# Kernel optimization log

Hardware: AMD Instinct MI355X
Metric: run time of the kernel (lower is better)

Reference implementation:

```python
import jax, jax.numpy as jnp
import numpy as np

N_NODES = 50000
N_EDGES = 800000
IN_CH = 128
HID = 128
NUM_CLASSES = 10
NUM_GRAPHS = 64


def _linear_params(key, fan_in, fan_out):
    kw, kb = jax.random.split(key)
    s = 1.0 / np.sqrt(fan_in)
    W = jax.random.uniform(kw, (fan_in, fan_out), jnp.float32, -s, s)
    b = jax.random.uniform(kb, (fan_out,), jnp.float32, -s, s)
    return W, b


def setup_inputs() -> dict:
    key = jax.random.key(0)
    ks = jax.random.split(key, 16)
    x = jax.random.normal(ks[0], (N_NODES, IN_CH), jnp.float32)
    edge_index = jax.random.randint(ks[1], (2, N_EDGES), 0, N_NODES, jnp.int64)
    batch = jnp.sort(jax.random.randint(ks[2], (N_NODES,), 0, NUM_GRAPHS, jnp.int64))
    inp = {"x": x, "edge_index": edge_index, "batch": batch}
    # conv layer 1 (in -> hid)
    inp["Wk1"], inp["bk1"] = _linear_params(ks[3], IN_CH, HID)
    inp["Wq1"], inp["bq1"] = _linear_params(ks[4], IN_CH, HID)
    inp["Wv1"], inp["bv1"] = _linear_params(ks[5], IN_CH, HID)
    inp["Ws1"], inp["bs1"] = _linear_params(ks[6], IN_CH, HID)
    inp["b1"] = jnp.zeros((HID,), jnp.float32)
    # conv layer 2 (hid -> hid)
    inp["Wk2"], inp["bk2"] = _linear_params(ks[7], HID, HID)
    inp["Wq2"], inp["bq2"] = _linear_params(ks[8], HID, HID)
    inp["Wv2"], inp["bv2"] = _linear_params(ks[9], HID, HID)
    inp["Ws2"], inp["bs2"] = _linear_params(ks[10], HID, HID)
    inp["b2"] = jnp.zeros((HID,), jnp.float32)
    # final fc
    inp["fcW"], inp["fcb"] = _linear_params(ks[11], HID, NUM_CLASSES)
    return inp


def _res_gated_conv(x, src, dst, Wk, bk, Wq, bq, Wv, bv, Ws, bs, b):
    # k from target node i, q and v from source node j (PyG ResGatedGraphConv)
    k = x @ Wk + bk            # [N, H]
    q = x @ Wq + bq            # [N, H]
    v = x @ Wv + bv            # [N, H]
    gate = jax.nn.sigmoid(k[dst] + q[src])   # [E, H]
    msg = gate * v[src]                       # [E, H]
    agg = jax.ops.segment_sum(msg, dst, num_segments=x.shape[0])
    return agg + x @ Ws + bs + b


def _global_mean_pool(x, batch, num_graphs):
    sums = jax.ops.segment_sum(x, batch, num_segments=num_graphs)
    cnts = jax.ops.segment_sum(jnp.ones((x.shape[0],), x.dtype), batch, num_segments=num_graphs)
    return sums / jnp.maximum(cnts, 1.0)[:, None]


def reference(x, edge_index, batch,
              Wk1, bk1, Wq1, bq1, Wv1, bv1, Ws1, bs1, b1,
              Wk2, bk2, Wq2, bq2, Wv2, bv2, Ws2, bs2, b2,
              fcW, fcb):
    src, dst = edge_index[0], edge_index[1]
    h = _res_gated_conv(x, src, dst, Wk1, bk1, Wq1, bq1, Wv1, bv1, Ws1, bs1, b1)
    h = jax.nn.relu(h)
    h = _res_gated_conv(h, src, dst, Wk2, bk2, Wq2, bq2, Wv2, bv2, Ws2, bs2, b2)
    h = jax.nn.relu(h)
    g = _global_mean_pool(h, batch, NUM_GRAPHS)   # [NUM_GRAPHS, HID]
    return g @ fcW + fcb                           # [NUM_GRAPHS, NUM_CLASSES]
```

## Files before the change

### kernel.cpp

```cpp
#include <hip/hip_runtime.h>
#include <math.h>


typedef __attribute__((ext_vector_type(8))) short short8;
typedef __attribute__((ext_vector_type(4))) float floatx4;
typedef __attribute__((ext_vector_type(8))) float floatx8;
typedef __attribute__((ext_vector_type(8))) unsigned short ushort8v;

__device__ __forceinline__ unsigned short f2b(float f) {
  unsigned int u = __builtin_bit_cast(unsigned int, f);
  u += 0x7fff + ((u >> 16) & 1);
  return (unsigned short)(u >> 16);
}
__device__ __forceinline__ float b2f(unsigned short u) {
  return __builtin_bit_cast(float, ((unsigned int)u) << 16);
}


__global__ __launch_bounds__(256) void hist_kernel(const int* __restrict__ dst,
                                                   int* __restrict__ cnt, int E) {
  int e = blockIdx.x * 256 + threadIdx.x;
  if (e < E) atomicAdd(&cnt[dst[e]], 1);
}

__global__ __launch_bounds__(256) void scan1_kernel(const int* __restrict__ cnt,
                                                    int* __restrict__ tmp_excl,
                                                    int* __restrict__ bsum, int n) {
  __shared__ int s[256];
  int t = threadIdx.x;
  int base = blockIdx.x * 512;
  int i0 = base + 2 * t, i1 = i0 + 1;
  int a0 = (i0 < n) ? cnt[i0] : 0;
  int a1 = (i1 < n) ? cnt[i1] : 0;
  int sum = a0 + a1;
  s[t] = sum;
  __syncthreads();
  for (int off = 1; off < 256; off <<= 1) {
    int v = (t >= off) ? s[t - off] : 0;
    __syncthreads();
    s[t] += v;
    __syncthreads();
  }
  int excl = s[t] - sum;
  if (i0 < n) tmp_excl[i0] = excl;
  if (i1 < n) tmp_excl[i1] = excl + a0;
  if (t == 255) bsum[blockIdx.x] = s[255];
}

__global__ __launch_bounds__(128) void scan2_kernel(const int* __restrict__ bsum,
                                                    int* __restrict__ boff, int nb) {
  __shared__ int s[128];
  int t = threadIdx.x;
  int v = (t < nb) ? bsum[t] : 0;
  s[t] = v;
  __syncthreads();
  for (int off = 1; off < 128; off <<= 1) {
    int u = (t >= off) ? s[t - off] : 0;
    __syncthreads();
    s[t] += u;
    __syncthreads();
  }
  if (t < nb) boff[t] = s[t] - v;
}

__global__ __launch_bounds__(256) void finalize_rp_kernel(const int* __restrict__ tmp_excl,
                                                          const int* __restrict__ boff,
                                                          int* __restrict__ row_ptr,
                                                          int* __restrict__ cursor,
                                                          int n, int E) {
  int i = blockIdx.x * 256 + threadIdx.x;
  if (i < n) {
    int v = tmp_excl[i] + boff[i >> 9];
    row_ptr[i] = v;
    cursor[i] = v;
  }
  if (i == 0) row_ptr[n] = E;
}

__global__ __launch_bounds__(256) void scatter_kernel(const int* __restrict__ src,
                                                      const int* __restrict__ dst,
                                                      int* __restrict__ cursor,
                                                      int* __restrict__ es, int E) {
  int e = blockIdx.x * 256 + threadIdx.x;
  if (e < E) {
    int i = dst[e];
    int p = atomicAdd(&cursor[i], 1);
    es[p] = src[e];
  }
}


__global__ __launch_bounds__(256) void convert_kernel(const float* __restrict__ X,
                                                      unsigned short* __restrict__ Xb,
                                                      int total4) {
  int i = blockIdx.x * 256 + threadIdx.x;
  if (i < total4) {
    float4 v = ((const float4*)X)[i];
    ushort4 o;
    o.x = f2b(v.x); o.y = f2b(v.y); o.z = f2b(v.z); o.w = f2b(v.w);
    ((ushort4*)Xb)[i] = o;
  }
}

__global__ __launch_bounds__(256) void prepack_w_kernel(
    const float* __restrict__ Wk1, const float* __restrict__ Wq1,
    const float* __restrict__ Wv1, const float* __restrict__ Ws1,
    const float* __restrict__ Wk2, const float* __restrict__ Wq2,
    const float* __restrict__ Wv2, const float* __restrict__ Ws2,
    unsigned short* __restrict__ WT) {
  int idx = blockIdx.x * 256 + threadIdx.x;
  int layer = idx >> 16;
  int rem = idx & 0xFFFF;
  int mat = rem >> 14;
  int nk = rem & 0x3FFF;
  int nn = nk >> 7, kk = nk & 127;
  int sel = layer * 4 + mat;
  const float* W = (sel == 0) ? Wk1 : (sel == 1) ? Wq1 : (sel == 2) ? Wv1 :
                   (sel == 3) ? Ws1 : (sel == 4) ? Wk2 : (sel == 5) ? Wq2 :
                   (sel == 6) ? Wv2 : Ws2;
  WT[idx] = f2b(W[kk * 128 + nn]);
}

__global__ __launch_bounds__(256) void prepack_b_kernel(
    const float* __restrict__ bk1, const float* __restrict__ bq1,
    const float* __restrict__ bv1, const float* __restrict__ bs1,
    const float* __restrict__ b1,
    const float* __restrict__ bk2, const float* __restrict__ bq2,
    const float* __restrict__ bv2, const float* __restrict__ bs2,
    const float* __restrict__ b2,
    float* __restrict__ bcat) {
  int idx = blockIdx.x * 256 + threadIdx.x;
  if (idx >= 1024) return;
  int layer = idx >> 9;
  int rem = idx & 511;
  int mat = rem >> 7, c = rem & 127;
  int sel = layer * 4 + mat;
  const float* b = (sel == 0) ? bk1 : (sel == 1) ? bq1 : (sel == 2) ? bv1 :
                   (sel == 3) ? bs1 : (sel == 4) ? bk2 : (sel == 5) ? bq2 :
                   (sel == 6) ? bv2 : bs2;
  float v = b[c];
  if (mat == 3) v += (layer == 0) ? b1[c] : b2[c];
  bcat[idx] = v;
}


__global__ __launch_bounds__(256) void gemm_mfma_kernel(
    const unsigned short* __restrict__ Xb,
    const unsigned short* __restrict__ WT,
    const float* __restrict__ bcat,
    unsigned short* __restrict__ Kb, unsigned short* __restrict__ Qb,
    unsigned short* __restrict__ Vb, float* __restrict__ S, int n) {
  __shared__ unsigned short aT[128 * 136];
  __shared__ float estage[4][16 * 68];

  int t = threadIdx.x;
  int row0 = blockIdx.x * 128;
  int m = blockIdx.y;

#pragma unroll
  for (int i = 0; i < 8; ++i) {
    int c = i * 256 + t;
    int r = c >> 4, col16 = c & 15;
    int4 v = make_int4(0, 0, 0, 0);
    if (row0 + r < n) v = *(const int4*)&Xb[(size_t)(row0 + r) * 128 + col16 * 8];
    *(int4*)&aT[r * 136 + col16 * 8] = v;
  }
  __syncthreads();

  int lane = t & 63, wid = t >> 6;
  int wy = wid >> 1, wx = wid & 1;
  int l15 = lane & 15, lq = lane >> 4;

  const unsigned short* WTm = WT + (size_t)m * 16384;

  floatx4 acc[4][4];
#pragma unroll
  for (int mf = 0; mf < 4; ++mf)
#pragma unroll
    for (int nf = 0; nf < 4; ++nf) acc[mf][nf] = (floatx4)(0.0f);

#pragma unroll
  for (int ks = 0; ks < 4; ++ks) {
    int kof = ks * 32 + lq * 8;
    short8 a[4], b[4];
#pragma unroll
    for (int mf = 0; mf < 4; ++mf)
      a[mf] = *(const short8*)&aT[(wy * 64 + mf * 16 + l15) * 136 + kof];
#pragma unroll
    for (int nf = 0; nf < 4; ++nf)
      b[nf] = *(const short8*)&WTm[(size_t)(wx * 64 + nf * 16 + l15) * 128 + kof];
#pragma unroll
    for (int mf = 0; mf < 4; ++mf)
#pragma unroll
      for (int nf = 0; nf < 4; ++nf)
        acc[mf][nf] = __builtin_amdgcn_mfma_f32_16x16x32_bf16(a[mf], b[nf], acc[mf][nf], 0, 0, 0);
  }

  const float* bias = bcat + m * 128;
  int r4 = lane >> 2, cq4 = lane & 3;
  int col = wx * 64 + cq4 * 16;
  float4 bv[4];
#pragma unroll
  for (int j = 0; j < 4; ++j) bv[j] = *(const float4*)&bias[col + j * 4];

  unsigned short* Ob = (m == 0) ? Kb : (m == 1) ? Qb : Vb;

#pragma unroll
  for (int mf = 0; mf < 4; ++mf) {
#pragma unroll
    for (int nf = 0; nf < 4; ++nf)
#pragma unroll
      for (int i = 0; i < 4; ++i)
        estage[wid][(lq * 4 + i) * 68 + nf * 16 + l15] = acc[mf][nf][i];
    int grow = row0 + wy * 64 + mf * 16 + r4;
    if (grow < n) {
      float4 p[4];
#pragma unroll
      for (int j = 0; j < 4; ++j) {
        float4 e = *(const float4*)&estage[wid][r4 * 68 + cq4 * 16 + j * 4];
        p[j].x = e.x + bv[j].x; p[j].y = e.y + bv[j].y;
        p[j].z = e.z + bv[j].z; p[j].w = e.w + bv[j].w;
      }
      if (m < 3) {
        ushort8v o0, o1;
        o0[0] = f2b(p[0].x); o0[1] = f2b(p[0].y); o0[2] = f2b(p[0].z); o0[3] = f2b(p[0].w);
        o0[4] = f2b(p[1].x); o0[5] = f2b(p[1].y); o0[6] = f2b(p[1].z); o0[7] = f2b(p[1].w);
        o1[0] = f2b(p[2].x); o1[1] = f2b(p[2].y); o1[2] = f2b(p[2].z); o1[3] = f2b(p[2].w);
        o1[4] = f2b(p[3].x); o1[5] = f2b(p[3].y); o1[6] = f2b(p[3].z); o1[7] = f2b(p[3].w);
        *(ushort8v*)&Ob[(size_t)grow * 128 + col] = o0;
        *(ushort8v*)&Ob[(size_t)grow * 128 + col + 8] = o1;
      } else {
#pragma unroll
        for (int j = 0; j < 4; ++j)
          *(float4*)&S[(size_t)grow * 128 + col + j * 4] = p[j];
      }
    }
  }
}


__global__ __launch_bounds__(256) void edge_agg_kernel(
    const unsigned short* __restrict__ Kb, const unsigned short* __restrict__ Qb,
    const unsigned short* __restrict__ Vb, const float* __restrict__ S,
    const int* __restrict__ row_ptr, const int* __restrict__ es,
    unsigned short* __restrict__ Hb, float* __restrict__ Hf, int mode, int n) {
  int wid = threadIdx.x >> 6;
  int lane = threadIdx.x & 63;
  int node = blockIdx.x * 4 + wid;
  if (node >= n) return;
  int grp = lane >> 4;
  int l16 = lane & 15;

  ushort8v kr = *(const ushort8v*)&Kb[(size_t)node * 128 + l16 * 8];
  float kc[8];
#pragma unroll
  for (int i = 0; i < 8; ++i) kc[i] = b2f(kr[i]);

  floatx8 acc = (floatx8)(0.0f);

  int e0 = row_ptr[node], e1 = row_ptr[node + 1];
  int e = e0 + grp;
  int j = (e < e1) ? es[e] : -1;
  while (j >= 0) {
    int en = e + 4;
    int jn = (en < e1) ? es[en] : -1;
    ushort8v q8 = *(const ushort8v*)&Qb[(size_t)j * 128 + l16 * 8];
    ushort8v v8 = *(const ushort8v*)&Vb[(size_t)j * 128 + l16 * 8];
#pragma unroll
    for (int i = 0; i < 8; ++i) {
      float q = b2f(q8[i]);
      float v = b2f(v8[i]);
      acc[i] += v / (1.0f + __expf(-(kc[i] + q)));
    }
    e = en; j = jn;
  }

#pragma unroll
  for (int i = 0; i < 8; ++i) {
    acc[i] += __shfl_xor(acc[i], 16);
    acc[i] += __shfl_xor(acc[i], 32);
  }

  if (grp == 0) {
    float4 s0 = *(const float4*)&S[(size_t)node * 128 + l16 * 8];
    float4 s1 = *(const float4*)&S[(size_t)node * 128 + l16 * 8 + 4];
    float r[8];
    r[0] = fmaxf(acc[0] + s0.x, 0.f); r[1] = fmaxf(acc[1] + s0.y, 0.f);
    r[2] = fmaxf(acc[2] + s0.z, 0.f); r[3] = fmaxf(acc[3] + s0.w, 0.f);
    r[4] = fmaxf(acc[4] + s1.x, 0.f); r[5] = fmaxf(acc[5] + s1.y, 0.f);
    r[6] = fmaxf(acc[6] + s1.z, 0.f); r[7] = fmaxf(acc[7] + s1.w, 0.f);
    if (mode == 0) {
      ushort8v o;
#pragma unroll
      for (int i = 0; i < 8; ++i) o[i] = f2b(r[i]);
      *(ushort8v*)&Hb[(size_t)node * 128 + l16 * 8] = o;
    } else {
      float4 h0 = make_float4(r[0], r[1], r[2], r[3]);
      float4 h1 = make_float4(r[4], r[5], r[6], r[7]);
      *(float4*)&Hf[(size_t)node * 128 + l16 * 8] = h0;
      *(float4*)&Hf[(size_t)node * 128 + l16 * 8 + 4] = h1;
    }
  }
}


__global__ __launch_bounds__(64) void graph_bounds_kernel(const int* __restrict__ batch,
                                                          int* __restrict__ gstart, int n) {
  int g = threadIdx.x;
  int lo = 0, hi = n;
  while (lo < hi) {
    int mid = (lo + hi) >> 1;
    if (batch[mid] < g) lo = mid + 1; else hi = mid;
  }
  gstart[g] = lo;
  if (g == 63) gstart[64] = n;
}

__global__ __launch_bounds__(256) void pool_sum_kernel(const float* __restrict__ Hf,
                                                       const int* __restrict__ gstart,
                                                       float* __restrict__ pool) {
  __shared__ float red[8 * 128];
  int g = blockIdx.x >> 4;
  int slice = blockIdx.x & 15;
  int t = threadIdx.x;
  int grp = t >> 5;
  int cq = t & 31;
  int s = gstart[g], e = gstart[g + 1];
  int cnt = e - s;
  int per = (cnt + 15) >> 4;
  int ss = s + slice * per;
  int ee = ss + per; if (ee > e) ee = e;

  float4 acc = make_float4(0.f, 0.f, 0.f, 0.f);
  const float4* H4 = (const float4*)Hf;
  for (int nd = ss + grp; nd < ee; nd += 8) {
    float4 v = H4[(size_t)nd * 32 + cq];
    acc.x += v.x; acc.y += v.y; acc.z += v.z; acc.w += v.w;
  }
  *(float4*)&red[grp * 128 + cq * 4] = acc;
  __syncthreads();
  if (t < 128) {
    float tot = 0.f;
#pragma unroll
    for (int g8 = 0; g8 < 8; ++g8) tot += red[g8 * 128 + t];
    if (tot != 0.f) atomicAdd(&pool[g * 128 + t], tot);
  }
}

__global__ __launch_bounds__(128) void fc_kernel(const float* __restrict__ pool,
                                                 const int* __restrict__ gstart,
                                                 const float* __restrict__ fcW,
                                                 const float* __restrict__ fcb,
                                                 float* __restrict__ out) {
  __shared__ float p[128];
  int g = blockIdx.x;
  int t = threadIdx.x;
  int cnt = gstart[g + 1] - gstart[g];
  float inv = 1.0f / (float)((cnt > 0) ? cnt : 1);
  p[t] = pool[g * 128 + t] * inv;
  __syncthreads();
  if (t < 10) {
    float s = fcb[t];
    for (int c = 0; c < 128; ++c) s += p[c] * fcW[c * 10 + t];
    out[g * 10 + t] = s;
  }
}


extern "C" void kernel_launch(void* const* d_in, const int* in_sizes, int n_in,
                              void* d_out, int out_size, void* d_ws, size_t ws_size,
                              hipStream_t stream) {
  const float* x   = (const float*)d_in[0];
  const int* eidx  = (const int*)d_in[1];
  const int* batch = (const int*)d_in[2];
  const float* Wk1 = (const float*)d_in[3];  const float* bk1 = (const float*)d_in[4];
  const float* Wq1 = (const float*)d_in[5];  const float* bq1 = (const float*)d_in[6];
  const float* Wv1 = (const float*)d_in[7];  const float* bv1 = (const float*)d_in[8];
  const float* Ws1 = (const float*)d_in[9];  const float* bs1 = (const float*)d_in[10];
  const float* b1  = (const float*)d_in[11];
  const float* Wk2 = (const float*)d_in[12]; const float* bk2 = (const float*)d_in[13];
  const float* Wq2 = (const float*)d_in[14]; const float* bq2 = (const float*)d_in[15];
  const float* Wv2 = (const float*)d_in[16]; const float* bv2 = (const float*)d_in[17];
  const float* Ws2 = (const float*)d_in[18]; const float* bs2 = (const float*)d_in[19];
  const float* b2  = (const float*)d_in[20];
  const float* fcW = (const float*)d_in[21]; const float* fcb = (const float*)d_in[22];
  float* out = (float*)d_out;

  const int N = in_sizes[0] / 128;
  const int E = in_sizes[1] / 2;
  const int* src = eidx;
  const int* dst = eidx + E;

  char* w = (char*)d_ws;
  size_t off = 0;
  auto carve = [&](size_t bytes) -> void* {
    void* p = w + off;
    off += (bytes + 255) & ~size_t(255);
    return p;
  };
  const size_t featB16 = (size_t)N * 128 * 2;
  const size_t featB32 = (size_t)N * 128 * 4;
  unsigned short* Xb = (unsigned short*)carve(featB16);
  unsigned short* Kb = (unsigned short*)carve(featB16);
  unsigned short* Qb = (unsigned short*)carve(featB16);
  unsigned short* Vb = (unsigned short*)carve(featB16);
  unsigned short* Hb = (unsigned short*)carve(featB16);
  float* S  = (float*)carve(featB32);
  float* Hf = (float*)carve(featB32);
  unsigned short* WT = (unsigned short*)carve(2 * 4 * 128 * 128 * 2);
  float* bcat = (float*)carve(1024 * 4);
  int* cnt      = (int*)carve((size_t)N * 4);
  int* row_ptr  = (int*)carve((size_t)(N + 1) * 4);
  int* cursor   = (int*)carve((size_t)N * 4);
  int* tmp_excl = (int*)carve((size_t)N * 4);
  int* bsum     = (int*)carve(256 * 4);
  int* boff     = (int*)carve(256 * 4);
  int* es       = (int*)carve((size_t)E * 4);
  int* gstart   = (int*)carve(65 * 4);
  float* pool   = (float*)carve(64 * 128 * 4);
  (void)ws_size; (void)n_in; (void)out_size;

  hipMemsetAsync(cnt, 0, (size_t)N * 4, stream);
  hipMemsetAsync(pool, 0, 64 * 128 * 4, stream);

  int nb512 = (N + 511) / 512;
  hist_kernel<<<(E + 255) / 256, 256, 0, stream>>>(dst, cnt, E);
  scan1_kernel<<<nb512, 256, 0, stream>>>(cnt, tmp_excl, bsum, N);
  scan2_kernel<<<1, 128, 0, stream>>>(bsum, boff, nb512);
  finalize_rp_kernel<<<(N + 255) / 256, 256, 0, stream>>>(tmp_excl, boff, row_ptr, cursor, N, E);
  scatter_kernel<<<(E + 255) / 256, 256, 0, stream>>>(src, dst, cursor, es, E);

  convert_kernel<<<(N * 32 + 255) / 256, 256, 0, stream>>>(x, Xb, N * 32);
  prepack_w_kernel<<<512, 256, 0, stream>>>(Wk1, Wq1, Wv1, Ws1, Wk2, Wq2, Wv2, Ws2, WT);
  prepack_b_kernel<<<4, 256, 0, stream>>>(bk1, bq1, bv1, bs1, b1,
                                          bk2, bq2, bv2, bs2, b2, bcat);

  dim3 ggrid((N + 127) / 128, 4);

  gemm_mfma_kernel<<<ggrid, 256, 0, stream>>>(Xb, WT, bcat, Kb, Qb, Vb, S, N);
  edge_agg_kernel<<<(N + 3) / 4, 256, 0, stream>>>(Kb, Qb, Vb, S, row_ptr, es,
                                                   Hb, Hf, 0, N);

  gemm_mfma_kernel<<<ggrid, 256, 0, stream>>>(Hb, WT + 65536, bcat + 512,
                                              Kb, Qb, Vb, S, N);
  edge_agg_kernel<<<(N + 3) / 4, 256, 0, stream>>>(Kb, Qb, Vb, S, row_ptr, es,
                                                   Hb, Hf, 1, N);

  graph_bounds_kernel<<<1, 64, 0, stream>>>(batch, gstart, N);
  pool_sum_kernel<<<1024, 256, 0, stream>>>(Hf, gstart, pool);
  fc_kernel<<<64, 128, 0, stream>>>(pool, gstart, fcW, fcb, out);
}
```

Measured before the change: 431.7 us.

## Merge prep kernels, drop graph bounds kernel, cheaper sigmoid, reuse LDS for staging

Merges the input conversion and weight/bias prepack kernels into one launch. The graph-bounds kernel is dropped and pool/fc now binary-search the batch array inline. The edge sigmoid uses exp2 with a pre-scaled key and a hardware reciprocal instead of a divide. The GEMM epilogue stages results in the A-tile LDS after a barrier instead of a separate buffer, which lowers LDS use and may raise occupancy. The aim is fewer launches and cheaper per-edge math, at the cost of redundant binary searches and a slightly less accurate reciprocal.

```diff
diff --git a/kernel.cpp b/kernel.cpp
--- a/kernel.cpp
+++ b/kernel.cpp
@@ -6,6 +6,8 @@
 typedef __attribute__((ext_vector_type(4))) float floatx4;
 typedef __attribute__((ext_vector_type(8))) float floatx8;
 typedef __attribute__((ext_vector_type(8))) unsigned short ushort8v;
+
+#define LOG2E 1.4426950408889634f
 
 __device__ __forceinline__ unsigned short f2b(float f) {
   unsigned int u = __builtin_bit_cast(unsigned int, f);
@@ -90,57 +92,61 @@
 }
 
 
-__global__ __launch_bounds__(256) void convert_kernel(const float* __restrict__ X,
-                                                      unsigned short* __restrict__ Xb,
-                                                      int total4) {
-  int i = blockIdx.x * 256 + threadIdx.x;
-  if (i < total4) {
-    float4 v = ((const float4*)X)[i];
-    ushort4 o;
-    o.x = f2b(v.x); o.y = f2b(v.y); o.z = f2b(v.z); o.w = f2b(v.w);
-    ((ushort4*)Xb)[i] = o;
-  }
-}
-
-__global__ __launch_bounds__(256) void prepack_w_kernel(
+__global__ __launch_bounds__(256) void prep_kernel(
+    const float* __restrict__ X, unsigned short* __restrict__ Xb, int total4,
     const float* __restrict__ Wk1, const float* __restrict__ Wq1,
     const float* __restrict__ Wv1, const float* __restrict__ Ws1,
     const float* __restrict__ Wk2, const float* __restrict__ Wq2,
     const float* __restrict__ Wv2, const float* __restrict__ Ws2,
-    unsigned short* __restrict__ WT) {
-  int idx = blockIdx.x * 256 + threadIdx.x;
-  int layer = idx >> 16;
-  int rem = idx & 0xFFFF;
-  int mat = rem >> 14;
-  int nk = rem & 0x3FFF;
-  int nn = nk >> 7, kk = nk & 127;
-  int sel = layer * 4 + mat;
-  const float* W = (sel == 0) ? Wk1 : (sel == 1) ? Wq1 : (sel == 2) ? Wv1 :
-                   (sel == 3) ? Ws1 : (sel == 4) ? Wk2 : (sel == 5) ? Wq2 :
-                   (sel == 6) ? Wv2 : Ws2;
-  WT[idx] = f2b(W[kk * 128 + nn]);
-}
-
-__global__ __launch_bounds__(256) void prepack_b_kernel(
+    unsigned short* __restrict__ WT,
     const float* __restrict__ bk1, const float* __restrict__ bq1,
     const float* __restrict__ bv1, const float* __restrict__ bs1,
     const float* __restrict__ b1,
     const float* __restrict__ bk2, const float* __restrict__ bq2,
     const float* __restrict__ bv2, const float* __restrict__ bs2,
     const float* __restrict__ b2,
-    float* __restrict__ bcat) {
-  int idx = blockIdx.x * 256 + threadIdx.x;
-  if (idx >= 1024) return;
-  int layer = idx >> 9;
-  int rem = idx & 511;
-  int mat = rem >> 7, c = rem & 127;
-  int sel = layer * 4 + mat;
-  const float* b = (sel == 0) ? bk1 : (sel == 1) ? bq1 : (sel == 2) ? bv1 :
-                   (sel == 3) ? bs1 : (sel == 4) ? bk2 : (sel == 5) ? bq2 :
-                   (sel == 6) ? bv2 : bs2;
-  float v = b[c];
-  if (mat == 3) v += (layer == 0) ? b1[c] : b2[c];
-  bcat[idx] = v;
+    float* __restrict__ bcat, int nconvb) {
+  int b = blockIdx.x;
+  if (b < nconvb) {
+    int i = b * 256 + threadIdx.x;
+    if (i < total4) {
+      float4 v = ((const float4*)X)[i];
+      ushort4 o;
+      o.x = f2b(v.x); o.y = f2b(v.y); o.z = f2b(v.z); o.w = f2b(v.w);
+      ((ushort4*)Xb)[i] = o;
+    }
+    return;
+  }
+  b -= nconvb;
+  if (b < 512) {
+    int idx = b * 256 + threadIdx.x;
+    int layer = idx >> 16;
+    int rem = idx & 0xFFFF;
+    int mat = rem >> 14;
+    int nk = rem & 0x3FFF;
+    int nn = nk >> 7, kk = nk & 127;
+    int sel = layer * 4 + mat;
+    const float* W = (sel == 0) ? Wk1 : (sel == 1) ? Wq1 : (sel == 2) ? Wv1 :
+                     (sel == 3) ? Ws1 : (sel == 4) ? Wk2 : (sel == 5) ? Wq2 :
+                     (sel == 6) ? Wv2 : Ws2;
+    WT[idx] = f2b(W[kk * 128 + nn]);
+    return;
+  }
+  b -= 512;
+  {
+    int idx = b * 256 + threadIdx.x;
+    if (idx >= 1024) return;
+    int layer = idx >> 9;
+    int rem = idx & 511;
+    int mat = rem >> 7, c = rem & 127;
+    int sel = layer * 4 + mat;
+    const float* bb = (sel == 0) ? bk1 : (sel == 1) ? bq1 : (sel == 2) ? bv1 :
+                      (sel == 3) ? bs1 : (sel == 4) ? bk2 : (sel == 5) ? bq2 :
+                      (sel == 6) ? bv2 : bs2;
+    float v = bb[c];
+    if (mat == 3) v += (layer == 0) ? b1[c] : b2[c];
+    bcat[idx] = v;
+  }
 }
 
 
@@ -151,7 +157,6 @@
     unsigned short* __restrict__ Kb, unsigned short* __restrict__ Qb,
     unsigned short* __restrict__ Vb, float* __restrict__ S, int n) {
   __shared__ unsigned short aT[128 * 136];
-  __shared__ float estage[4][16 * 68];
 
   int t = threadIdx.x;
   int row0 = blockIdx.x * 128;
@@ -196,6 +201,9 @@
         acc[mf][nf] = __builtin_amdgcn_mfma_f32_16x16x32_bf16(a[mf], b[nf], acc[mf][nf], 0, 0, 0);
   }
 
+  __syncthreads();
+  float* estage = (float*)aT + (size_t)wid * 1088;
+
   const float* bias = bcat + m * 128;
   int r4 = lane >> 2, cq4 = lane & 3;
   int col = wx * 64 + cq4 * 16;
@@ -211,13 +219,13 @@
     for (int nf = 0; nf < 4; ++nf)
 #pragma unroll
       for (int i = 0; i < 4; ++i)
-        estage[wid][(lq * 4 + i) * 68 + nf * 16 + l15] = acc[mf][nf][i];
+        estage[(lq * 4 + i) * 68 + nf * 16 + l15] = acc[mf][nf][i];
     int grow = row0 + wy * 64 + mf * 16 + r4;
     if (grow < n) {
       float4 p[4];
 #pragma unroll
       for (int j = 0; j < 4; ++j) {
-        float4 e = *(const float4*)&estage[wid][r4 * 68 + cq4 * 16 + j * 4];
+        float4 e = *(const float4*)&estage[r4 * 68 + cq4 * 16 + j * 4];
         p[j].x = e.x + bv[j].x; p[j].y = e.y + bv[j].y;
         p[j].z = e.z + bv[j].z; p[j].w = e.w + bv[j].w;
       }
@@ -252,9 +260,9 @@
   int l16 = lane & 15;
 
   ushort8v kr = *(const ushort8v*)&Kb[(size_t)node * 128 + l16 * 8];
-  float kc[8];
-#pragma unroll
-  for (int i = 0; i < 8; ++i) kc[i] = b2f(kr[i]);
+  float kcn[8];
+#pragma unroll
+  for (int i = 0; i < 8; ++i) kcn[i] = b2f(kr[i]) * (-LOG2E);
 
   floatx8 acc = (floatx8)(0.0f);
 
@@ -270,7 +278,8 @@
     for (int i = 0; i < 8; ++i) {
       float q = b2f(q8[i]);
       float v = b2f(v8[i]);
-      acc[i] += v / (1.0f + __expf(-(kc[i] + q)));
+      float ex = __builtin_amdgcn_exp2f(fmaf(q, -LOG2E, kcn[i]));
+      acc[i] = fmaf(v, __builtin_amdgcn_rcpf(1.0f + ex), acc[i]);
     }
     e = en; j = jn;
   }
@@ -304,28 +313,25 @@
 }
 
 
-__global__ __launch_bounds__(64) void graph_bounds_kernel(const int* __restrict__ batch,
-                                                          int* __restrict__ gstart, int n) {
-  int g = threadIdx.x;
+__device__ __forceinline__ int lb_batch(const int* __restrict__ batch, int n, int key) {
   int lo = 0, hi = n;
   while (lo < hi) {
     int mid = (lo + hi) >> 1;
-    if (batch[mid] < g) lo = mid + 1; else hi = mid;
-  }
-  gstart[g] = lo;
-  if (g == 63) gstart[64] = n;
+    if (batch[mid] < key) lo = mid + 1; else hi = mid;
+  }
+  return lo;
 }
 
 __global__ __launch_bounds__(256) void pool_sum_kernel(const float* __restrict__ Hf,
-                                                       const int* __restrict__ gstart,
-                                                       float* __restrict__ pool) {
+                                                       const int* __restrict__ batch,
+                                                       float* __restrict__ pool, int n) {
   __shared__ float red[8 * 128];
   int g = blockIdx.x >> 4;
   int slice = blockIdx.x & 15;
   int t = threadIdx.x;
   int grp = t >> 5;
   int cq = t & 31;
-  int s = gstart[g], e = gstart[g + 1];
+  int s = lb_batch(batch, n, g), e = lb_batch(batch, n, g + 1);
   int cnt = e - s;
   int per = (cnt + 15) >> 4;
   int ss = s + slice * per;
@@ -348,14 +354,14 @@
 }
 
 __global__ __launch_bounds__(128) void fc_kernel(const float* __restrict__ pool,
-                                                 const int* __restrict__ gstart,
+                                                 const int* __restrict__ batch,
                                                  const float* __restrict__ fcW,
                                                  const float* __restrict__ fcb,
-                                                 float* __restrict__ out) {
+                                                 float* __restrict__ out, int n) {
   __shared__ float p[128];
   int g = blockIdx.x;
   int t = threadIdx.x;
-  int cnt = gstart[g + 1] - gstart[g];
+  int cnt = lb_batch(batch, n, g + 1) - lb_batch(batch, n, g);
   float inv = 1.0f / (float)((cnt > 0) ? cnt : 1);
   p[t] = pool[g * 128 + t] * inv;
   __syncthreads();
@@ -416,7 +422,6 @@
   int* bsum     = (int*)carve(256 * 4);
   int* boff     = (int*)carve(256 * 4);
   int* es       = (int*)carve((size_t)E * 4);
-  int* gstart   = (int*)carve(65 * 4);
   float* pool   = (float*)carve(64 * 128 * 4);
   (void)ws_size; (void)n_in; (void)out_size;
 
@@ -430,10 +435,11 @@
   finalize_rp_kernel<<<(N + 255) / 256, 256, 0, stream>>>(tmp_excl, boff, row_ptr, cursor, N, E);
   scatter_kernel<<<(E + 255) / 256, 256, 0, stream>>>(src, dst, cursor, es, E);
 
-  convert_kernel<<<(N * 32 + 255) / 256, 256, 0, stream>>>(x, Xb, N * 32);
-  prepack_w_kernel<<<512, 256, 0, stream>>>(Wk1, Wq1, Wv1, Ws1, Wk2, Wq2, Wv2, Ws2, WT);
-  prepack_b_kernel<<<4, 256, 0, stream>>>(bk1, bq1, bv1, bs1, b1,
-                                          bk2, bq2, bv2, bs2, b2, bcat);
+  int nconvb = (N * 32 + 255) / 256;
+  prep_kernel<<<nconvb + 512 + 4, 256, 0, stream>>>(
+      x, Xb, N * 32,
+      Wk1, Wq1, Wv1, Ws1, Wk2, Wq2, Wv2, Ws2, WT,
+      bk1, bq1, bv1, bs1, b1, bk2, bq2, bv2, bs2, b2, bcat, nconvb);
 
   dim3 ggrid((N + 127) / 128, 4);
 
@@ -446,7 +452,6 @@
   edge_agg_kernel<<<(N + 3) / 4, 256, 0, stream>>>(Kb, Qb, Vb, S, row_ptr, es,
                                                    Hb, Hf, 1, N);
 
-  graph_bounds_kernel<<<1, 64, 0, stream>>>(batch, gstart, N);
-  pool_sum_kernel<<<1024, 256, 0, stream>>>(Hf, gstart, pool);
-  fc_kernel<<<64, 128, 0, stream>>>(pool, gstart, fcW, fcb, out);
-}
+  pool_sum_kernel<<<1024, 256, 0, stream>>>(Hf, batch, pool, N);
+  fc_kernel<<<64, 128, 0, stream>>>(pool, batch, fcW, fcb, out, N);
+}
```

Result: no change. 427.6 us (-0.9%).
